# Optimization experiments

Hardware: AMD Instinct MI355X
Metric: run time of the kernel (lower is better)

## Reference

```python
import jax, jax.numpy as jnp
import numpy as np

N = 100000
F_IN = 256
F_OUT = 128
E = 1600000


def setup_inputs() -> dict:
    key = jax.random.key(0)
    k1, k2, k3, k4 = jax.random.split(key, 4)
    x = jax.random.normal(k1, (N, F_IN), dtype=jnp.float32)
    edge_index = jax.random.randint(k2, (2, E), 0, N, dtype=jnp.int64)
    # GCNConv parameters (glorot-ish init) + PReLU per-channel slope (torch default 0.25)
    W = jax.random.normal(k3, (F_IN, F_OUT), dtype=jnp.float32) / np.sqrt(F_IN)
    bias = jnp.zeros((F_OUT,), dtype=jnp.float32)
    prelu_a = jnp.full((F_OUT,), 0.25, dtype=jnp.float32)
    return {"x": x, "edge_index": edge_index, "W": W, "bias": bias, "prelu_a": prelu_a}


def reference(x, edge_index, W, bias, prelu_a):
    n = x.shape[0]
    # PyG GCNConv: linear transform first
    h = x @ W  # [N, F_OUT]
    # add self-loops (GCNConv default add_self_loops=True)
    loop = jnp.arange(n, dtype=edge_index.dtype)
    row = jnp.concatenate([edge_index[0], loop])  # source
    col = jnp.concatenate([edge_index[1], loop])  # target
    # symmetric degree normalization: deg over targets with unit edge weights
    ones = jnp.ones(row.shape[0], dtype=h.dtype)
    deg = jax.ops.segment_sum(ones, col, num_segments=n)
    deg_inv_sqrt = jnp.where(deg > 0, jax.lax.rsqrt(deg), 0.0)
    norm = deg_inv_sqrt[row] * deg_inv_sqrt[col]  # [E+N]
    # gather-normalize-scatter aggregation
    msgs = h[row] * norm[:, None]  # [E+N, F_OUT]
    out = jax.ops.segment_sum(msgs, col, num_segments=n) + bias  # [N, F_OUT]
    # PReLU with per-channel slope
    z = jnp.where(out > 0, out, prelu_a * out)
    return z
```

## Files before the change

### kernel.cpp

```cpp
#include <hip/hip_runtime.h>

#define N_NODES 100000
#define F_IN    256
#define F_OUT   128
#define N_EDGES 1600000

#define BSH       8
#define NBUCK     ((N_NODES + 255) >> 8)
#define ECAP      4608
#define CPAD      16
#define K3_BLOCKS 250
#define K3_Q      (N_EDGES / 4 / K3_BLOCKS)

typedef unsigned int   uint;
typedef unsigned char  uchar;
typedef unsigned short ushort;
typedef short  s16x8 __attribute__((ext_vector_type(8)));
typedef float  f32x4 __attribute__((ext_vector_type(4)));

__device__ __forceinline__ ushort f2bf(float f) {
    uint b = __float_as_uint(f);
    b += 0x7FFFu + ((b >> 16) & 1u);
    return (ushort)(b >> 16);
}
__device__ __forceinline__ float bf2f(uint h16) {
    return __uint_as_float(h16 << 16);
}

__global__ __launch_bounds__(256) void wpack_kernel(const float* __restrict__ W,
                                                    ushort* __restrict__ Wp,
                                                    int* __restrict__ gcur) {
    const int gid = blockIdx.x * 256 + threadIdx.x;
    for (int i = gid; i < NBUCK * CPAD; i += 4096) gcur[i] = 0;

    const int lane = gid & 63;
    const int s    = (gid >> 6) & 7;
    const int t    = gid >> 9;
    const int krow = s * 32 + (lane >> 4) * 8;
    const int col  = t * 16 + (lane & 15);
    ushort h[8];
#pragma unroll
    for (int j = 0; j < 8; ++j)
        h[j] = f2bf(W[(krow + j) * F_OUT + col]);
    ushort* dst = &Wp[(size_t)gid * 8];
#pragma unroll
    for (int j = 0; j < 8; ++j) dst[j] = h[j];
}

__global__ __launch_bounds__(256) void bscatter_kernel(const int* __restrict__ ei,
                                                       int* __restrict__ gcur,
                                                       int* __restrict__ ebuf) {
    __shared__ __align__(16) int tv[K3_Q * 4];
    __shared__ int h[NBUCK];
    for (int i = threadIdx.x; i < NBUCK; i += 256) h[i] = 0;
    __syncthreads();
    const int g0 = blockIdx.x * K3_Q;
    const int4* tgt = (const int4*)&ei[N_EDGES];
    const int4* src = (const int4*)&ei[0];
    for (int q = threadIdx.x; q < K3_Q; q += 256) {
        const int4 v = tgt[g0 + q];
        atomicAdd(&h[v.x >> BSH], 1);
        atomicAdd(&h[v.y >> BSH], 1);
        atomicAdd(&h[v.z >> BSH], 1);
        atomicAdd(&h[v.w >> BSH], 1);
        *(int4*)&tv[q * 4] = v;
    }
    __syncthreads();
    for (int i = threadIdx.x; i < NBUCK; i += 256) {
        const int c = h[i];
        h[i] = c ? atomicAdd(&gcur[i * CPAD], c) : 0;
    }
    __syncthreads();
    for (int q = threadIdx.x; q < K3_Q; q += 256) {
        const int4 u = src[g0 + q];
        const int4 v = *(const int4*)&tv[q * 4];
        const int b0 = v.x >> BSH, b1 = v.y >> BSH, b2 = v.z >> BSH, b3 = v.w >> BSH;
        const int s0 = atomicAdd(&h[b0], 1);
        const int s1 = atomicAdd(&h[b1], 1);
        const int s2 = atomicAdd(&h[b2], 1);
        const int s3 = atomicAdd(&h[b3], 1);
        if (s0 < ECAP) ebuf[b0 * ECAP + s0] = ((v.x & 255) << 17) | u.x;
        if (s1 < ECAP) ebuf[b1 * ECAP + s1] = ((v.y & 255) << 17) | u.y;
        if (s2 < ECAP) ebuf[b2 * ECAP + s2] = ((v.z & 255) << 17) | u.z;
        if (s3 < ECAP) ebuf[b3 * ECAP + s3] = ((v.w & 255) << 17) | u.w;
    }
}

__global__ __launch_bounds__(256) void build_kernel(const int* __restrict__ gcur,
                                                    const int* __restrict__ ebuf,
                                                    int* __restrict__ adj,
                                                    int* __restrict__ count,
                                                    int* __restrict__ off,
                                                    float* __restrict__ dinv) {
    __shared__ int cnt[256];
    __shared__ int scan[256];
    const int b  = blockIdx.x;
    const int t  = threadIdx.x;
    int ec = gcur[b * CPAD];
    ec = ec < ECAP ? ec : ECAP;
    const int e0 = b * ECAP;
    cnt[t] = 0;
    __syncthreads();
    for (int i = t; i < ec; i += 256)
        atomicAdd(&cnt[(ebuf[e0 + i] >> 17) & 255], 1);
    __syncthreads();
    const int val = cnt[t];
    scan[t] = val;
    __syncthreads();
    for (int o = 1; o < 256; o <<= 1) {
        const int add = (t >= o) ? scan[t - o] : 0;
        __syncthreads();
        scan[t] += add;
        __syncthreads();
    }
    const int excl = scan[t] - val;
    const int v = (b << BSH) + t;
    if (v < N_NODES) {
        off[v]   = e0 + excl;
        count[v] = val;
        dinv[v]  = rsqrtf((float)(val + 1));
    }
    cnt[t] = excl;
    __syncthreads();
    for (int i = t; i < ec; i += 256) {
        const int key  = ebuf[e0 + i];
        const int slot = atomicAdd(&cnt[(key >> 17) & 255], 1);
        adj[e0 + slot] = key & 0x1FFFF;
    }
}

__global__ __launch_bounds__(256) void mfma_gemm_kernel(const float* __restrict__ x,
                                                        const s16x8* __restrict__ Wp,
                                                        const float* __restrict__ dinv,
                                                        ushort* __restrict__ g16) {
    const int tid  = threadIdx.x;
    const int wave = tid >> 6;
    const int lane = tid & 63;
    const int aq   = lane >> 4;
    const int al   = lane & 15;

    const int row_base = blockIdx.x * 64 + wave * 16;
    const int arow = row_base + al;
    const int arow_c = arow < N_NODES ? arow : N_NODES - 1;
    const float* xrow = &x[(size_t)arow_c * F_IN + aq * 8];

    f32x4 acc[8] = {};

#pragma unroll
    for (int s = 0; s < 8; ++s) {
        const float4 a0 = *(const float4*)&xrow[s * 32];
        const float4 a1 = *(const float4*)&xrow[s * 32 + 4];
        s16x8 af;
        af[0] = (short)f2bf(a0.x); af[1] = (short)f2bf(a0.y);
        af[2] = (short)f2bf(a0.z); af[3] = (short)f2bf(a0.w);
        af[4] = (short)f2bf(a1.x); af[5] = (short)f2bf(a1.y);
        af[6] = (short)f2bf(a1.z); af[7] = (short)f2bf(a1.w);
#pragma unroll
        for (int t = 0; t < 8; ++t) {
            const s16x8 bf = Wp[(t * 8 + s) * 64 + lane];
            acc[t] = __builtin_amdgcn_mfma_f32_16x16x32_bf16(af, bf, acc[t], 0, 0, 0);
        }
    }

    const int rrow0 = row_base + aq * 4;
    const float4 dv = *(const float4*)&dinv[rrow0];
    const float dvr[4] = {dv.x, dv.y, dv.z, dv.w};
#pragma unroll
    for (int r = 0; r < 4; ++r) {
        const int row = rrow0 + r;
        if (row < N_NODES) {
            ushort* orow = &g16[(size_t)row * F_OUT];
#pragma unroll
            for (int t = 0; t < 8; ++t)
                orow[t * 16 + al] = f2bf(acc[t][r] * dvr[r]);
        }
    }
}

#define ACC8(r) \
    a0 += __uint_as_float((r).x << 16); a1 += __uint_as_float((r).x & 0xFFFF0000u); \
    a2 += __uint_as_float((r).y << 16); a3 += __uint_as_float((r).y & 0xFFFF0000u); \
    a4 += __uint_as_float((r).z << 16); a5 += __uint_as_float((r).z & 0xFFFF0000u); \
    a6 += __uint_as_float((r).w << 16); a7 += __uint_as_float((r).w & 0xFFFF0000u);

__global__ __launch_bounds__(256) void aggregate_kernel(const int* __restrict__ count,
                                                        const int* __restrict__ off,
                                                        const float* __restrict__ dinv,
                                                        const int* __restrict__ adj,
                                                        const ushort* __restrict__ g16,
                                                        const float* __restrict__ bias,
                                                        const float* __restrict__ prelu_a,
                                                        float* __restrict__ out) {
    const int tid = threadIdx.x;
    const int l   = tid & 15;
    const int v   = blockIdx.x * 16 + (tid >> 4);
    if (v >= N_NODES) return;
    const int f   = l * 8;

    const uint4 sv = *(const uint4*)&g16[(uint)v * F_OUT + f];
    float a0 = bf2f(sv.x & 0xFFFFu), a1 = __uint_as_float(sv.x & 0xFFFF0000u);
    float a2 = bf2f(sv.y & 0xFFFFu), a3 = __uint_as_float(sv.y & 0xFFFF0000u);
    float a4 = bf2f(sv.z & 0xFFFFu), a5 = __uint_as_float(sv.z & 0xFFFF0000u);
    float a6 = bf2f(sv.w & 0xFFFFu), a7 = __uint_as_float(sv.w & 0xFFFF0000u);

    const int c = count[v];
    const int* adj_v = &adj[off[v]];

    int i = 0;
    for (; i + 8 <= c; i += 8) {
        const int u0 = adj_v[i + 0], u1 = adj_v[i + 1], u2 = adj_v[i + 2], u3 = adj_v[i + 3];
        const int u4 = adj_v[i + 4], u5 = adj_v[i + 5], u6 = adj_v[i + 6], u7 = adj_v[i + 7];
        const uint4 r0 = *(const uint4*)&g16[(uint)u0 * F_OUT + f];
        const uint4 r1 = *(const uint4*)&g16[(uint)u1 * F_OUT + f];
        const uint4 r2 = *(const uint4*)&g16[(uint)u2 * F_OUT + f];
        const uint4 r3 = *(const uint4*)&g16[(uint)u3 * F_OUT + f];
        const uint4 r4 = *(const uint4*)&g16[(uint)u4 * F_OUT + f];
        const uint4 r5 = *(const uint4*)&g16[(uint)u5 * F_OUT + f];
        const uint4 r6 = *(const uint4*)&g16[(uint)u6 * F_OUT + f];
        const uint4 r7 = *(const uint4*)&g16[(uint)u7 * F_OUT + f];
        ACC8(r0); ACC8(r1); ACC8(r2); ACC8(r3);
        ACC8(r4); ACC8(r5); ACC8(r6); ACC8(r7);
    }
    for (; i + 4 <= c; i += 4) {
        const int u0 = adj_v[i + 0], u1 = adj_v[i + 1], u2 = adj_v[i + 2], u3 = adj_v[i + 3];
        const uint4 r0 = *(const uint4*)&g16[(uint)u0 * F_OUT + f];
        const uint4 r1 = *(const uint4*)&g16[(uint)u1 * F_OUT + f];
        const uint4 r2 = *(const uint4*)&g16[(uint)u2 * F_OUT + f];
        const uint4 r3 = *(const uint4*)&g16[(uint)u3 * F_OUT + f];
        ACC8(r0); ACC8(r1); ACC8(r2); ACC8(r3);
    }
    for (; i + 2 <= c; i += 2) {
        const int u0 = adj_v[i + 0], u1 = adj_v[i + 1];
        const uint4 r0 = *(const uint4*)&g16[(uint)u0 * F_OUT + f];
        const uint4 r1 = *(const uint4*)&g16[(uint)u1 * F_OUT + f];
        ACC8(r0); ACC8(r1);
    }
    if (i < c) {
        const int u0 = adj_v[i];
        const uint4 r0 = *(const uint4*)&g16[(uint)u0 * F_OUT + f];
        ACC8(r0);
    }

    const float s = dinv[v];
    const float4 bi0 = *(const float4*)&bias[f];
    const float4 bi1 = *(const float4*)&bias[f + 4];
    const float4 pa0 = *(const float4*)&prelu_a[f];
    const float4 pa1 = *(const float4*)&prelu_a[f + 4];
    float4 o0, o1;
    o0.x = a0 * s + bi0.x;  o0.y = a1 * s + bi0.y;
    o0.z = a2 * s + bi0.z;  o0.w = a3 * s + bi0.w;
    o1.x = a4 * s + bi1.x;  o1.y = a5 * s + bi1.y;
    o1.z = a6 * s + bi1.z;  o1.w = a7 * s + bi1.w;
    o0.x = o0.x > 0.f ? o0.x : pa0.x * o0.x;
    o0.y = o0.y > 0.f ? o0.y : pa0.y * o0.y;
    o0.z = o0.z > 0.f ? o0.z : pa0.z * o0.z;
    o0.w = o0.w > 0.f ? o0.w : pa0.w * o0.w;
    o1.x = o1.x > 0.f ? o1.x : pa1.x * o1.x;
    o1.y = o1.y > 0.f ? o1.y : pa1.y * o1.y;
    o1.z = o1.z > 0.f ? o1.z : pa1.z * o1.z;
    o1.w = o1.w > 0.f ? o1.w : pa1.w * o1.w;
    *(float4*)&out[(uint)v * F_OUT + f]     = o0;
    *(float4*)&out[(uint)v * F_OUT + f + 4] = o1;
}

extern "C" void kernel_launch(void* const* d_in, const int* in_sizes, int n_in,
                              void* d_out, int out_size, void* d_ws, size_t ws_size,
                              hipStream_t stream) {
    const float* x    = (const float*)d_in[0];
    const int*   ei   = (const int*)d_in[1];
    const float* W    = (const float*)d_in[2];
    const float* bias = (const float*)d_in[3];
    const float* pa   = (const float*)d_in[4];
    float* out = (float*)d_out;

    char* ws = (char*)d_ws;
    int*    count = (int*)ws;
    float*  dinv  = (float*)(ws + 400384);
    int*    off   = (int*)(ws + 800768);
    int*    gcur  = (int*)(ws + 1201152);
    int*    adj   = (int*)(ws + 1226240);
    ushort* g16   = (ushort*)(ws + 8433152);
    int*    ebuf  = (int*)(ws + 8433152);
    ushort* Wp    = (ushort*)(ws + 34033152);

    wpack_kernel<<<16, 256, 0, stream>>>(W, Wp, gcur);
    bscatter_kernel<<<K3_BLOCKS, 256, 0, stream>>>(ei, gcur, ebuf);
    build_kernel<<<NBUCK, 256, 0, stream>>>(gcur, ebuf, adj, count, off, dinv);
    mfma_gemm_kernel<<<(N_NODES + 63) / 64, 256, 0, stream>>>(x, (const s16x8*)Wp, dinv, g16);
    aggregate_kernel<<<(N_NODES + 15) / 16, 256, 0, stream>>>(count, off, dinv, adj, g16, bias, pa, out);
}
```

Before: 288.6 us.

## Fuse edge bucketing with GEMM in one launch and apply source norm during aggregation

Edge bucket-scatter blocks and MFMA GEMM blocks now share one launch, so the memory-bound scatter and the compute-heavy GEMM can overlap on the device. To allow this, the source-side degree scaling moves out of the GEMM epilogue into the aggregation loop, which now gathers dinv[u] per neighbor and accumulates with FMA. The edge buffer gets its own workspace region instead of aliasing g16. The scatter block count doubles and build_kernel runs 512 threads. In exchange, aggregation does an extra scattered 4-byte load per edge, and the fused kernel's LDS footprint applies to the GEMM blocks too, which may limit their occupancy.

```diff
diff --git a/kernel.cpp b/kernel.cpp
--- a/kernel.cpp
+++ b/kernel.cpp
@@ -9,8 +9,9 @@
 #define NBUCK     ((N_NODES + 255) >> 8)
 #define ECAP      4608
 #define CPAD      16
-#define K3_BLOCKS 250
-#define K3_Q      (N_EDGES / 4 / K3_BLOCKS)
+#define SCAT_BLOCKS 500
+#define SCAT_Q    (N_EDGES / 4 / SCAT_BLOCKS)
+#define GEMM_BLOCKS ((N_NODES + 63) / 64)
 
 typedef unsigned int   uint;
 typedef unsigned char  uchar;
@@ -47,46 +48,94 @@
     for (int j = 0; j < 8; ++j) dst[j] = h[j];
 }
 
-__global__ __launch_bounds__(256) void bscatter_kernel(const int* __restrict__ ei,
-                                                       int* __restrict__ gcur,
-                                                       int* __restrict__ ebuf) {
-    __shared__ __align__(16) int tv[K3_Q * 4];
+__global__ __launch_bounds__(256) void fused_kernel(const int* __restrict__ ei,
+                                                    int* __restrict__ gcur,
+                                                    int* __restrict__ ebuf,
+                                                    const float* __restrict__ x,
+                                                    const s16x8* __restrict__ Wp,
+                                                    ushort* __restrict__ g16) {
+    __shared__ __align__(16) int tv[SCAT_Q * 4];
     __shared__ int h[NBUCK];
-    for (int i = threadIdx.x; i < NBUCK; i += 256) h[i] = 0;
-    __syncthreads();
-    const int g0 = blockIdx.x * K3_Q;
-    const int4* tgt = (const int4*)&ei[N_EDGES];
-    const int4* src = (const int4*)&ei[0];
-    for (int q = threadIdx.x; q < K3_Q; q += 256) {
-        const int4 v = tgt[g0 + q];
-        atomicAdd(&h[v.x >> BSH], 1);
-        atomicAdd(&h[v.y >> BSH], 1);
-        atomicAdd(&h[v.z >> BSH], 1);
-        atomicAdd(&h[v.w >> BSH], 1);
-        *(int4*)&tv[q * 4] = v;
-    }
-    __syncthreads();
-    for (int i = threadIdx.x; i < NBUCK; i += 256) {
-        const int c = h[i];
-        h[i] = c ? atomicAdd(&gcur[i * CPAD], c) : 0;
-    }
-    __syncthreads();
-    for (int q = threadIdx.x; q < K3_Q; q += 256) {
-        const int4 u = src[g0 + q];
-        const int4 v = *(const int4*)&tv[q * 4];
-        const int b0 = v.x >> BSH, b1 = v.y >> BSH, b2 = v.z >> BSH, b3 = v.w >> BSH;
-        const int s0 = atomicAdd(&h[b0], 1);
-        const int s1 = atomicAdd(&h[b1], 1);
-        const int s2 = atomicAdd(&h[b2], 1);
-        const int s3 = atomicAdd(&h[b3], 1);
-        if (s0 < ECAP) ebuf[b0 * ECAP + s0] = ((v.x & 255) << 17) | u.x;
-        if (s1 < ECAP) ebuf[b1 * ECAP + s1] = ((v.y & 255) << 17) | u.y;
-        if (s2 < ECAP) ebuf[b2 * ECAP + s2] = ((v.z & 255) << 17) | u.z;
-        if (s3 < ECAP) ebuf[b3 * ECAP + s3] = ((v.w & 255) << 17) | u.w;
-    }
-}
-
-__global__ __launch_bounds__(256) void build_kernel(const int* __restrict__ gcur,
+
+    if (blockIdx.x < SCAT_BLOCKS) {
+        for (int i = threadIdx.x; i < NBUCK; i += 256) h[i] = 0;
+        __syncthreads();
+        const int g0 = blockIdx.x * SCAT_Q;
+        const int4* tgt = (const int4*)&ei[N_EDGES];
+        const int4* src = (const int4*)&ei[0];
+        for (int q = threadIdx.x; q < SCAT_Q; q += 256) {
+            const int4 v = tgt[g0 + q];
+            atomicAdd(&h[v.x >> BSH], 1);
+            atomicAdd(&h[v.y >> BSH], 1);
+            atomicAdd(&h[v.z >> BSH], 1);
+            atomicAdd(&h[v.w >> BSH], 1);
+            *(int4*)&tv[q * 4] = v;
+        }
+        __syncthreads();
+        for (int i = threadIdx.x; i < NBUCK; i += 256) {
+            const int c = h[i];
+            h[i] = c ? atomicAdd(&gcur[i * CPAD], c) : 0;
+        }
+        __syncthreads();
+        for (int q = threadIdx.x; q < SCAT_Q; q += 256) {
+            const int4 u = src[g0 + q];
+            const int4 v = *(const int4*)&tv[q * 4];
+            const int b0 = v.x >> BSH, b1 = v.y >> BSH, b2 = v.z >> BSH, b3 = v.w >> BSH;
+            const int s0 = atomicAdd(&h[b0], 1);
+            const int s1 = atomicAdd(&h[b1], 1);
+            const int s2 = atomicAdd(&h[b2], 1);
+            const int s3 = atomicAdd(&h[b3], 1);
+            if (s0 < ECAP) ebuf[b0 * ECAP + s0] = ((v.x & 255) << 17) | u.x;
+            if (s1 < ECAP) ebuf[b1 * ECAP + s1] = ((v.y & 255) << 17) | u.y;
+            if (s2 < ECAP) ebuf[b2 * ECAP + s2] = ((v.z & 255) << 17) | u.z;
+            if (s3 < ECAP) ebuf[b3 * ECAP + s3] = ((v.w & 255) << 17) | u.w;
+        }
+    } else {
+        const int bid  = blockIdx.x - SCAT_BLOCKS;
+        const int tid  = threadIdx.x;
+        const int wave = tid >> 6;
+        const int lane = tid & 63;
+        const int aq   = lane >> 4;
+        const int al   = lane & 15;
+
+        const int row_base = bid * 64 + wave * 16;
+        const int arow = row_base + al;
+        const int arow_c = arow < N_NODES ? arow : N_NODES - 1;
+        const float* xrow = &x[(size_t)arow_c * F_IN + aq * 8];
+
+        f32x4 acc[8] = {};
+
+#pragma unroll
+        for (int s = 0; s < 8; ++s) {
+            const float4 a0 = *(const float4*)&xrow[s * 32];
+            const float4 a1 = *(const float4*)&xrow[s * 32 + 4];
+            s16x8 af;
+            af[0] = (short)f2bf(a0.x); af[1] = (short)f2bf(a0.y);
+            af[2] = (short)f2bf(a0.z); af[3] = (short)f2bf(a0.w);
+            af[4] = (short)f2bf(a1.x); af[5] = (short)f2bf(a1.y);
+            af[6] = (short)f2bf(a1.z); af[7] = (short)f2bf(a1.w);
+#pragma unroll
+            for (int t = 0; t < 8; ++t) {
+                const s16x8 bf = Wp[(t * 8 + s) * 64 + lane];
+                acc[t] = __builtin_amdgcn_mfma_f32_16x16x32_bf16(af, bf, acc[t], 0, 0, 0);
+            }
+        }
+
+        const int rrow0 = row_base + aq * 4;
+#pragma unroll
+        for (int r = 0; r < 4; ++r) {
+            const int row = rrow0 + r;
+            if (row < N_NODES) {
+                ushort* orow = &g16[(size_t)row * F_OUT];
+#pragma unroll
+                for (int t = 0; t < 8; ++t)
+                    orow[t * 16 + al] = f2bf(acc[t][r]);
+            }
+        }
+    }
+}
+
+__global__ __launch_bounds__(512) void build_kernel(const int* __restrict__ gcur,
                                                     const int* __restrict__ ebuf,
                                                     int* __restrict__ adj,
                                                     int* __restrict__ count,
@@ -99,89 +148,48 @@
     int ec = gcur[b * CPAD];
     ec = ec < ECAP ? ec : ECAP;
     const int e0 = b * ECAP;
-    cnt[t] = 0;
+    if (t < 256) cnt[t] = 0;
     __syncthreads();
-    for (int i = t; i < ec; i += 256)
+    for (int i = t; i < ec; i += 512)
         atomicAdd(&cnt[(ebuf[e0 + i] >> 17) & 255], 1);
     __syncthreads();
-    const int val = cnt[t];
-    scan[t] = val;
+    const int val = (t < 256) ? cnt[t] : 0;
+    if (t < 256) scan[t] = val;
     __syncthreads();
     for (int o = 1; o < 256; o <<= 1) {
-        const int add = (t >= o) ? scan[t - o] : 0;
-        __syncthreads();
-        scan[t] += add;
-        __syncthreads();
-    }
-    const int excl = scan[t] - val;
-    const int v = (b << BSH) + t;
-    if (v < N_NODES) {
-        off[v]   = e0 + excl;
-        count[v] = val;
-        dinv[v]  = rsqrtf((float)(val + 1));
-    }
-    cnt[t] = excl;
+        int add = 0;
+        if (t < 256 && t >= o) add = scan[t - o];
+        __syncthreads();
+        if (t < 256) scan[t] += add;
+        __syncthreads();
+    }
+    if (t < 256) {
+        const int excl = scan[t] - val;
+        const int v = (b << BSH) + t;
+        if (v < N_NODES) {
+            off[v]   = e0 + excl;
+            count[v] = val;
+            dinv[v]  = rsqrtf((float)(val + 1));
+        }
+        cnt[t] = excl;
+    }
     __syncthreads();
-    for (int i = t; i < ec; i += 256) {
+    for (int i = t; i < ec; i += 512) {
         const int key  = ebuf[e0 + i];
         const int slot = atomicAdd(&cnt[(key >> 17) & 255], 1);
         adj[e0 + slot] = key & 0x1FFFF;
     }
 }
 
-__global__ __launch_bounds__(256) void mfma_gemm_kernel(const float* __restrict__ x,
-                                                        const s16x8* __restrict__ Wp,
-                                                        const float* __restrict__ dinv,
-                                                        ushort* __restrict__ g16) {
-    const int tid  = threadIdx.x;
-    const int wave = tid >> 6;
-    const int lane = tid & 63;
-    const int aq   = lane >> 4;
-    const int al   = lane & 15;
-
-    const int row_base = blockIdx.x * 64 + wave * 16;
-    const int arow = row_base + al;
-    const int arow_c = arow < N_NODES ? arow : N_NODES - 1;
-    const float* xrow = &x[(size_t)arow_c * F_IN + aq * 8];
-
-    f32x4 acc[8] = {};
-
-#pragma unroll
-    for (int s = 0; s < 8; ++s) {
-        const float4 a0 = *(const float4*)&xrow[s * 32];
-        const float4 a1 = *(const float4*)&xrow[s * 32 + 4];
-        s16x8 af;
-        af[0] = (short)f2bf(a0.x); af[1] = (short)f2bf(a0.y);
-        af[2] = (short)f2bf(a0.z); af[3] = (short)f2bf(a0.w);
-        af[4] = (short)f2bf(a1.x); af[5] = (short)f2bf(a1.y);
-        af[6] = (short)f2bf(a1.z); af[7] = (short)f2bf(a1.w);
-#pragma unroll
-        for (int t = 0; t < 8; ++t) {
-            const s16x8 bf = Wp[(t * 8 + s) * 64 + lane];
-            acc[t] = __builtin_amdgcn_mfma_f32_16x16x32_bf16(af, bf, acc[t], 0, 0, 0);
-        }
-    }
-
-    const int rrow0 = row_base + aq * 4;
-    const float4 dv = *(const float4*)&dinv[rrow0];
-    const float dvr[4] = {dv.x, dv.y, dv.z, dv.w};
-#pragma unroll
-    for (int r = 0; r < 4; ++r) {
-        const int row = rrow0 + r;
-        if (row < N_NODES) {
-            ushort* orow = &g16[(size_t)row * F_OUT];
-#pragma unroll
-            for (int t = 0; t < 8; ++t)
-                orow[t * 16 + al] = f2bf(acc[t][r] * dvr[r]);
-        }
-    }
-}
-
-#define ACC8(r) \
-    a0 += __uint_as_float((r).x << 16); a1 += __uint_as_float((r).x & 0xFFFF0000u); \
-    a2 += __uint_as_float((r).y << 16); a3 += __uint_as_float((r).y & 0xFFFF0000u); \
-    a4 += __uint_as_float((r).z << 16); a5 += __uint_as_float((r).z & 0xFFFF0000u); \
-    a6 += __uint_as_float((r).w << 16); a7 += __uint_as_float((r).w & 0xFFFF0000u);
+#define FMA8(r, d) \
+    a0 = fmaf(d, __uint_as_float((r).x << 16),        a0); \
+    a1 = fmaf(d, __uint_as_float((r).x & 0xFFFF0000u), a1); \
+    a2 = fmaf(d, __uint_as_float((r).y << 16),        a2); \
+    a3 = fmaf(d, __uint_as_float((r).y & 0xFFFF0000u), a3); \
+    a4 = fmaf(d, __uint_as_float((r).z << 16),        a4); \
+    a5 = fmaf(d, __uint_as_float((r).z & 0xFFFF0000u), a5); \
+    a6 = fmaf(d, __uint_as_float((r).w << 16),        a6); \
+    a7 = fmaf(d, __uint_as_float((r).w & 0xFFFF0000u), a7);
 
 __global__ __launch_bounds__(256) void aggregate_kernel(const int* __restrict__ count,
                                                         const int* __restrict__ off,
@@ -197,11 +205,12 @@
     if (v >= N_NODES) return;
     const int f   = l * 8;
 
+    const float s = dinv[v];
     const uint4 sv = *(const uint4*)&g16[(uint)v * F_OUT + f];
-    float a0 = bf2f(sv.x & 0xFFFFu), a1 = __uint_as_float(sv.x & 0xFFFF0000u);
-    float a2 = bf2f(sv.y & 0xFFFFu), a3 = __uint_as_float(sv.y & 0xFFFF0000u);
-    float a4 = bf2f(sv.z & 0xFFFFu), a5 = __uint_as_float(sv.z & 0xFFFF0000u);
-    float a6 = bf2f(sv.w & 0xFFFFu), a7 = __uint_as_float(sv.w & 0xFFFF0000u);
+    float a0 = s * bf2f(sv.x & 0xFFFFu), a1 = s * __uint_as_float(sv.x & 0xFFFF0000u);
+    float a2 = s * bf2f(sv.y & 0xFFFFu), a3 = s * __uint_as_float(sv.y & 0xFFFF0000u);
+    float a4 = s * bf2f(sv.z & 0xFFFFu), a5 = s * __uint_as_float(sv.z & 0xFFFF0000u);
+    float a6 = s * bf2f(sv.w & 0xFFFFu), a7 = s * __uint_as_float(sv.w & 0xFFFF0000u);
 
     const int c = count[v];
     const int* adj_v = &adj[off[v]];
@@ -210,6 +219,8 @@
     for (; i + 8 <= c; i += 8) {
         const int u0 = adj_v[i + 0], u1 = adj_v[i + 1], u2 = adj_v[i + 2], u3 = adj_v[i + 3];
         const int u4 = adj_v[i + 4], u5 = adj_v[i + 5], u6 = adj_v[i + 6], u7 = adj_v[i + 7];
+        const float d0 = dinv[u0], d1 = dinv[u1], d2 = dinv[u2], d3 = dinv[u3];
+        const float d4 = dinv[u4], d5 = dinv[u5], d6 = dinv[u6], d7 = dinv[u7];
         const uint4 r0 = *(const uint4*)&g16[(uint)u0 * F_OUT + f];
         const uint4 r1 = *(const uint4*)&g16[(uint)u1 * F_OUT + f];
         const uint4 r2 = *(const uint4*)&g16[(uint)u2 * F_OUT + f];
@@ -218,30 +229,32 @@
         const uint4 r5 = *(const uint4*)&g16[(uint)u5 * F_OUT + f];
         const uint4 r6 = *(const uint4*)&g16[(uint)u6 * F_OUT + f];
         const uint4 r7 = *(const uint4*)&g16[(uint)u7 * F_OUT + f];
-        ACC8(r0); ACC8(r1); ACC8(r2); ACC8(r3);
-        ACC8(r4); ACC8(r5); ACC8(r6); ACC8(r7);
+        FMA8(r0, d0); FMA8(r1, d1); FMA8(r2, d2); FMA8(r3, d3);
+        FMA8(r4, d4); FMA8(r5, d5); FMA8(r6, d6); FMA8(r7, d7);
     }
     for (; i + 4 <= c; i += 4) {
         const int u0 = adj_v[i + 0], u1 = adj_v[i + 1], u2 = adj_v[i + 2], u3 = adj_v[i + 3];
+        const float d0 = dinv[u0], d1 = dinv[u1], d2 = dinv[u2], d3 = dinv[u3];
         const uint4 r0 = *(const uint4*)&g16[(uint)u0 * F_OUT + f];
         const uint4 r1 = *(const uint4*)&g16[(uint)u1 * F_OUT + f];
         const uint4 r2 = *(const uint4*)&g16[(uint)u2 * F_OUT + f];
         const uint4 r3 = *(const uint4*)&g16[(uint)u3 * F_OUT + f];
-        ACC8(r0); ACC8(r1); ACC8(r2); ACC8(r3);
+        FMA8(r0, d0); FMA8(r1, d1); FMA8(r2, d2); FMA8(r3, d3);
     }
     for (; i + 2 <= c; i += 2) {
         const int u0 = adj_v[i + 0], u1 = adj_v[i + 1];
+        const float d0 = dinv[u0], d1 = dinv[u1];
         const uint4 r0 = *(const uint4*)&g16[(uint)u0 * F_OUT + f];
         const uint4 r1 = *(const uint4*)&g16[(uint)u1 * F_OUT + f];
-        ACC8(r0); ACC8(r1);
+        FMA8(r0, d0); FMA8(r1, d1);
     }
     if (i < c) {
         const int u0 = adj_v[i];
+        const float d0 = dinv[u0];
         const uint4 r0 = *(const uint4*)&g16[(uint)u0 * F_OUT + f];
-        ACC8(r0);
-    }
-
-    const float s = dinv[v];
+        FMA8(r0, d0);
+    }
+
     const float4 bi0 = *(const float4*)&bias[f];
     const float4 bi1 = *(const float4*)&bias[f + 4];
     const float4 pa0 = *(const float4*)&prelu_a[f];
@@ -280,12 +293,12 @@
     int*    gcur  = (int*)(ws + 1201152);
     int*    adj   = (int*)(ws + 1226240);
     ushort* g16   = (ushort*)(ws + 8433152);
-    int*    ebuf  = (int*)(ws + 8433152);
-    ushort* Wp    = (ushort*)(ws + 34033152);
+    int*    ebuf  = (int*)(ws + 34033152);
+    ushort* Wp    = (ushort*)(ws + 41240064);
 
     wpack_kernel<<<16, 256, 0, stream>>>(W, Wp, gcur);
-    bscatter_kernel<<<K3_BLOCKS, 256, 0, stream>>>(ei, gcur, ebuf);
-    build_kernel<<<NBUCK, 256, 0, stream>>>(gcur, ebuf, adj, count, off, dinv);
-    mfma_gemm_kernel<<<(N_NODES + 63) / 64, 256, 0, stream>>>(x, (const s16x8*)Wp, dinv, g16);
+    fused_kernel<<<SCAT_BLOCKS + GEMM_BLOCKS, 256, 0, stream>>>(ei, gcur, ebuf,
+                                                                x, (const s16x8*)Wp, g16);
+    build_kernel<<<NBUCK, 512, 0, stream>>>(gcur, ebuf, adj, count, off, dinv);
     aggregate_kernel<<<(N_NODES + 15) / 16, 256, 0, stream>>>(count, off, dinv, adj, g16, bias, pa, out);
 }
```

Measured after the change: 291.1 us. Within noise of the previous version (+0.8%).
